# Optimization experiments

Measured on AMD Instinct MI355X. Metric: run time of the kernel, lower is better.

## Reference

```python
import jax, jax.numpy as jnp
import numpy as np

DIM = 768
HEADS = 12
DH = DIM // HEADS
HID = 4 * DIM
EPS = 1e-5


def _layernorm(y, g, b):
    mu = jnp.mean(y, axis=-1, keepdims=True)
    var = jnp.mean(jnp.square(y - mu), axis=-1, keepdims=True)
    return (y - mu) * jax.lax.rsqrt(var + EPS) * g + b


def setup_inputs() -> dict:
    key = jax.random.key(0)
    ks = jax.random.split(key, 8)
    s = 0.02
    return {
        "x": jax.random.normal(ks[0], (8, 1024, DIM), dtype=jnp.float32),
        "Wqkv": jax.random.normal(ks[1], (DIM, 3 * DIM), dtype=jnp.float32) * s,
        "bqkv": jnp.zeros((3 * DIM,), jnp.float32),
        "Wproj": jax.random.normal(ks[2], (DIM, DIM), dtype=jnp.float32) * s,
        "bproj": jnp.zeros((DIM,), jnp.float32),
        "W1": jax.random.normal(ks[3], (DIM, HID), dtype=jnp.float32) * s,
        "b1": jnp.zeros((HID,), jnp.float32),
        "W2": jax.random.normal(ks[4], (HID, DIM), dtype=jnp.float32) * s,
        "b2": jnp.zeros((DIM,), jnp.float32),
        "g1": jnp.ones((DIM,), jnp.float32),
        "be1": jnp.zeros((DIM,), jnp.float32),
        "g2": jnp.ones((DIM,), jnp.float32),
        "be2": jnp.zeros((DIM,), jnp.float32),
    }


def reference(x, Wqkv, bqkv, Wproj, bproj, W1, b1, W2, b2, g1, be1, g2, be2):
    b, n, d = x.shape
    # QKV projection; source splits last dim as (h, d_head, qkv) -> qkv innermost
    qkv = (x @ Wqkv + bqkv).reshape(b, n, HEADS, DH, 3)
    q, k, v = qkv[..., 0], qkv[..., 1], qkv[..., 2]  # [b, n, h, dh]
    scores = jnp.einsum('bqhd,bkhd->bhqk', q, k)
    # NOTE: source applies the 1/sqrt(dim) scale AFTER softmax (quirk preserved)
    attn = jax.nn.softmax(scores, axis=-1) / (d ** 0.5)
    out = jnp.einsum('bhqk,bkhd->bqhd', attn, v).reshape(b, n, d)
    attn_out = out @ Wproj + bproj
    # Residual with norm on the branch output (not pre-norm), per source
    x = x + _layernorm(attn_out, g1, be1)
    mlp_out = jax.nn.gelu(x @ W1 + b1, approximate=False) @ W2 + b2
    return x + _layernorm(mlp_out, g2, be2)
```

## Files before the change

### kernel.cpp

```cpp
#include <hip/hip_runtime.h>
#include <math.h>

typedef float f32x4 __attribute__((ext_vector_type(4)));
typedef short s16x8 __attribute__((ext_vector_type(8)));

#define DIM_ 768
#define HEADS_ 12
#define DH_ 64
#define HID_ 3072
#define SEQ_ 1024
#define BATCH_ 8
#define ROWS_ (BATCH_*SEQ_)

static __device__ __forceinline__ ushort f2bf(float f) {
    union { float f; unsigned u; } v; v.f = f;
    unsigned r = (v.u + 0x7fffu + ((v.u >> 16) & 1u)) >> 16;
    return (ushort)r;
}
static __device__ __forceinline__ float bf2f(ushort u) {
    union { unsigned u; float f; } v; v.u = ((unsigned)u) << 16;
    return v.f;
}

static __device__ __forceinline__ void glds16(const ushort* gp, ushort* lp) {
    __builtin_amdgcn_global_load_lds(
        (const __attribute__((address_space(1))) void*)gp,
        (__attribute__((address_space(3))) void*)lp, 16, 0, 0);
}

__global__ __launch_bounds__(256) void cast_bf16_kernel(
    const float* __restrict__ in, ushort* __restrict__ out, int n4)
{
    int i = blockIdx.x * 256 + threadIdx.x;
    if (i >= n4) return;
    float4 v = ((const float4*)in)[i];
    ushort4 o;
    o.x = f2bf(v.x); o.y = f2bf(v.y); o.z = f2bf(v.z); o.w = f2bf(v.w);
    ((ushort4*)out)[i] = o;
}

__global__ __launch_bounds__(256) void transpose_cast_kernel(
    const float* __restrict__ W, ushort* __restrict__ WT, int K, int N)
{
    __shared__ float tile[32][33];
    int n0 = blockIdx.x * 32, k0 = blockIdx.y * 32;
    int tx = threadIdx.x, ty = threadIdx.y;
#pragma unroll
    for (int i = 0; i < 4; i++)
        tile[ty + i * 8][tx] = W[(size_t)(k0 + ty + i * 8) * N + n0 + tx];
    __syncthreads();
#pragma unroll
    for (int i = 0; i < 4; i++)
        WT[(size_t)(n0 + ty + i * 8) * K + k0 + tx] = f2bf(tile[tx][ty + i * 8]);
}

#define EPI_PART 0
#define EPI_GELU 1
#define EPI_QKV 2

template<int EPI>
__global__ __launch_bounds__(256, 3) void gemm_bt(
    const ushort* __restrict__ A, const ushort* __restrict__ B,
    const float* __restrict__ bias,
    ushort* __restrict__ Cp,
    ushort* __restrict__ Qb, ushort* __restrict__ Kb, ushort* __restrict__ Vt,
    int M, int N, int K, int nx, int nk, int Ksl)
{
    __shared__ ushort As[128 * 64];
    __shared__ ushort Bs[128 * 64];
    const int t = threadIdx.x;
    const int lane = t & 63;
    const int w = t >> 6;
    const int wr = w >> 1, wc = w & 1;
    const int nwg = gridDim.x;
    const int chunk = nwg >> 3;
    const int lin = (blockIdx.x & 7) * chunk + (blockIdx.x >> 3);
    const int tile = lin / nk;
    const int ks = lin - tile * nk;
    const int m0 = (tile / nx) * 128, n0 = (tile % nx) * 128;
    const int lr = lane & 15, g = lane >> 4;

    const ushort* Ak = A + (size_t)ks * Ksl;
    const ushort* Bk = B + (size_t)ks * Ksl;
    const int sr = lane >> 3;
    const int scz = (((lane & 7) ^ sr)) * 8;

    f32x4 acc[4][4] = {};

    for (int k0 = 0; k0 < Ksl; k0 += 64) {
#pragma unroll
        for (int j = 0; j < 4; j++) {
            int r = w * 32 + j * 8;
            glds16(Ak + (size_t)(m0 + r + sr) * K + k0 + scz, &As[r * 64]);
            glds16(Bk + (size_t)(n0 + r + sr) * K + k0 + scz, &Bs[r * 64]);
        }
        __syncthreads();
#pragma unroll
        for (int kk = 0; kk < 2; kk++) {
            s16x8 af[4], bfr[4];
#pragma unroll
            for (int m = 0; m < 4; m++) {
                int row = wr * 64 + m * 16 + lr;
                int slot = (kk * 4 + g) ^ (row & 7);
                af[m] = *(const s16x8*)&As[row * 64 + slot * 8];
            }
#pragma unroll
            for (int n = 0; n < 4; n++) {
                int row = wc * 64 + n * 16 + lr;
                int slot = (kk * 4 + g) ^ (row & 7);
                bfr[n] = *(const s16x8*)&Bs[row * 64 + slot * 8];
            }
#pragma unroll
            for (int m = 0; m < 4; m++)
#pragma unroll
                for (int n = 0; n < 4; n++)
                    acc[m][n] = __builtin_amdgcn_mfma_f32_16x16x32_bf16(af[m], bfr[n], acc[m][n], 0, 0, 0);
        }
        __syncthreads();
    }

    ushort* Cpo = Cp ? Cp + (size_t)ks * M * N : nullptr;
#pragma unroll
    for (int m = 0; m < 4; m++) {
        int row = m0 + wr * 64 + m * 16 + g * 4;
#pragma unroll
        for (int n = 0; n < 4; n++) {
            int col = n0 + wc * 64 + n * 16 + lr;
            float bv = (ks == 0) ? bias[col] : 0.f;
#pragma unroll
            for (int r = 0; r < 4; r++) {
                float v = acc[m][n][r] + bv;
                int rg = row + r;
                if (EPI == EPI_PART) {
                    Cpo[(size_t)rg * N + col] = f2bf(v);
                } else if (EPI == EPI_GELU) {
                    float u = v * (0.7978845608f + 0.0356774081f * v * v);
                    float th = 1.f - 2.f / (__expf(2.f * u) + 1.f);
                    float gl = 0.5f * v * (1.f + th);
                    Cpo[(size_t)rg * N + col] = f2bf(gl);
                } else {
                    int b = rg >> 10, nrow = rg & 1023;
                    int h = col / 192, rem = col % 192;
                    int dh = rem / 3, wh = rem % 3;
                    int hb = b * HEADS_ + h;
                    ushort bw = f2bf(v);
                    if (wh == 0)      Qb[((size_t)hb * SEQ_ + nrow) * DH_ + dh] = bw;
                    else if (wh == 1) Kb[((size_t)hb * SEQ_ + nrow) * DH_ + dh] = bw;
                    else              Vt[(size_t)hb * DH_ * SEQ_ + (size_t)dh * SEQ_ + nrow] = bw;
                }
            }
        }
    }
}

static __device__ __forceinline__ void pack_pv(
    const f32x4 (&S)[4], s16x8& pf0v, s16x8& pf1v)
{
    unsigned c[4][2];
#pragma unroll
    for (int n = 0; n < 4; n++) {
        asm("v_cvt_pk_bf16_f32 %0, %1, %2" : "=v"(c[n][0]) : "v"(S[n][0]), "v"(S[n][1]));
        asm("v_cvt_pk_bf16_f32 %0, %1, %2" : "=v"(c[n][1]) : "v"(S[n][2]), "v"(S[n][3]));
    }
    union { unsigned u[4]; s16x8 v; } pf0, pf1;
#pragma unroll
    for (int m = 0; m < 2; m++) {
        unsigned a = c[0][m], bb = c[1][m];
        asm("v_permlane32_swap_b32 %0, %1" : "+v"(a), "+v"(bb));
        asm("v_permlane16_swap_b32 %0, %1" : "+v"(a), "+v"(bb));
        pf0.u[m] = a; pf0.u[2 + m] = bb;
        unsigned a2 = c[2][m], b2 = c[3][m];
        asm("v_permlane32_swap_b32 %0, %1" : "+v"(a2), "+v"(b2));
        asm("v_permlane16_swap_b32 %0, %1" : "+v"(a2), "+v"(b2));
        pf1.u[m] = a2; pf1.u[2 + m] = b2;
    }
    pf0v = pf0.v; pf1v = pf1.v;
}

struct AttnState {
    s16x8 aqA0, aqA1, aqB0, aqB1;
    float lA, lB;
    f32x4 OA[4], OB[4];
};

static __device__ __forceinline__ void attn_tile_lds(
    AttnState& st, const ushort* Ksb, const ushort* Vsb, int lr, int g)
{
    const float CMAX = 20.f;
    const int x = lr & 7;
    s16x8 kf[8], vf[8];
#pragma unroll
    for (int n = 0; n < 4; n++) {
        int row = n * 16 + lr;
        kf[2 * n]     = *(const s16x8*)&Ksb[row * 64 + (g ^ x) * 8];
        kf[2 * n + 1] = *(const s16x8*)&Ksb[row * 64 + ((4 + g) ^ x) * 8];
        vf[2 * n]     = *(const s16x8*)&Vsb[row * 64 + (g ^ x) * 8];
        vf[2 * n + 1] = *(const s16x8*)&Vsb[row * 64 + ((4 + g) ^ x) * 8];
    }
    f32x4 SA[4] = {}, SB[4] = {};
#pragma unroll
    for (int n = 0; n < 4; n++) {
        SA[n] = __builtin_amdgcn_mfma_f32_16x16x32_bf16(kf[2 * n], st.aqA0, SA[n], 0, 0, 0);
        SA[n] = __builtin_amdgcn_mfma_f32_16x16x32_bf16(kf[2 * n + 1], st.aqA1, SA[n], 0, 0, 0);
    }
#pragma unroll
    for (int n = 0; n < 4; n++) {
        SB[n] = __builtin_amdgcn_mfma_f32_16x16x32_bf16(kf[2 * n], st.aqB0, SB[n], 0, 0, 0);
        SB[n] = __builtin_amdgcn_mfma_f32_16x16x32_bf16(kf[2 * n + 1], st.aqB1, SB[n], 0, 0, 0);
    }
#pragma unroll
    for (int n = 0; n < 4; n++)
#pragma unroll
        for (int r = 0; r < 4; r++) {
            SA[n][r] = __expf(SA[n][r] - CMAX);
            SB[n][r] = __expf(SB[n][r] - CMAX);
        }
    f32x4 sa = SA[0] + SA[1], sb = SB[0] + SB[1];
    sa += SA[2] + SA[3];
    sb += SB[2] + SB[3];
    st.lA += (sa[0] + sa[1]) + (sa[2] + sa[3]);
    st.lB += (sb[0] + sb[1]) + (sb[2] + sb[3]);

    s16x8 pfA0, pfA1, pfB0, pfB1;
    pack_pv(SA, pfA0, pfA1);
    pack_pv(SB, pfB0, pfB1);

#pragma unroll
    for (int n = 0; n < 4; n++) {
        st.OA[n] = __builtin_amdgcn_mfma_f32_16x16x32_bf16(pfA0, vf[2 * n], st.OA[n], 0, 0, 0);
        st.OA[n] = __builtin_amdgcn_mfma_f32_16x16x32_bf16(pfA1, vf[2 * n + 1], st.OA[n], 0, 0, 0);
    }
#pragma unroll
    for (int n = 0; n < 4; n++) {
        st.OB[n] = __builtin_amdgcn_mfma_f32_16x16x32_bf16(pfB0, vf[2 * n], st.OB[n], 0, 0, 0);
        st.OB[n] = __builtin_amdgcn_mfma_f32_16x16x32_bf16(pfB1, vf[2 * n + 1], st.OB[n], 0, 0, 0);
    }
}

__global__ __launch_bounds__(256) void attn_kernel(
    const ushort* __restrict__ Q, const ushort* __restrict__ Kb,
    const ushort* __restrict__ Vt, ushort* __restrict__ AO)
{
    __shared__ ushort Ks[2][64 * 64];
    __shared__ ushort Vs[2][64 * 64];
    const int tid = threadIdx.x, lane = tid & 63, w = tid >> 6;
    const int lr = lane & 15, g = lane >> 4;
    const int wg = blockIdx.x;
    const int lin = (wg & 7) * 96 + (wg >> 3);
    const int bh = lin >> 3;
    const int qt = lin & 7;
    const int b = bh / HEADS_, h = bh % HEADS_;
    const ushort* qh = Q + (size_t)bh * SEQ_ * DH_;
    const ushort* kh = Kb + (size_t)bh * SEQ_ * DH_;
    const ushort* vh = Vt + (size_t)bh * DH_ * SEQ_;

    const int srow = tid >> 3;
    const int ss = (tid & 7) ^ (srow & 7);

    AttnState st;
    const int qbase = qt * 128 + w * 32;
    st.aqA0 = *(const s16x8*)(qh + (size_t)(qbase + lr) * DH_ + g * 8);
    st.aqA1 = *(const s16x8*)(qh + (size_t)(qbase + lr) * DH_ + 32 + g * 8);
    st.aqB0 = *(const s16x8*)(qh + (size_t)(qbase + 16 + lr) * DH_ + g * 8);
    st.aqB1 = *(const s16x8*)(qh + (size_t)(qbase + 16 + lr) * DH_ + 32 + g * 8);
    st.lA = 0.f; st.lB = 0.f;
#pragma unroll
    for (int n = 0; n < 4; n++) { st.OA[n] = f32x4{}; st.OB[n] = f32x4{}; }

    auto stageK = [&](ushort* buf, int kbase) {
        glds16(kh + (size_t)(kbase + srow) * DH_ + ss * 8, &buf[tid * 8]);
        glds16(kh + (size_t)(kbase + 32 + srow) * DH_ + ss * 8, &buf[tid * 8 + 2048]);
    };
    auto stageV = [&](ushort* buf, int kbase) {
        glds16(vh + (size_t)srow * SEQ_ + kbase + ss * 8, &buf[tid * 8]);
        glds16(vh + (size_t)(32 + srow) * SEQ_ + kbase + ss * 8, &buf[tid * 8 + 2048]);
    };

    stageK(Ks[0], 0);
    stageV(Vs[0], 0);
    __syncthreads();

#pragma unroll 1
    for (int tkv = 0; tkv < 16; tkv += 2) {
        if (tkv + 1 < 16) { stageK(Ks[1], (tkv + 1) * 64); stageV(Vs[1], (tkv + 1) * 64); }
        attn_tile_lds(st, Ks[0], Vs[0], lr, g);
        __syncthreads();
        if (tkv + 2 < 16) { stageK(Ks[0], (tkv + 2) * 64); stageV(Vs[0], (tkv + 2) * 64); }
        attn_tile_lds(st, Ks[1], Vs[1], lr, g);
        __syncthreads();
    }

    float lA = st.lA, lB = st.lB;
    lA += __shfl_xor(lA, 16); lA += __shfl_xor(lA, 32);
    lB += __shfl_xor(lB, 16); lB += __shfl_xor(lB, 32);

    const float fin = 0.03608439182435161f;
#pragma unroll
    for (int r = 0; r < 4; r++) {
        float linvA = fin / __shfl(lA, 4 * g + r);
        float linvB = fin / __shfl(lB, 4 * g + r);
        int rowA = b * SEQ_ + qbase + 4 * g + r;
        int rowB = rowA + 16;
        ushort* aoA = AO + (size_t)rowA * DIM_ + h * DH_ + lr;
        ushort* aoB = AO + (size_t)rowB * DIM_ + h * DH_ + lr;
#pragma unroll
        for (int n = 0; n < 4; n++) {
            aoA[n * 16] = f2bf(st.OA[n][r] * linvA);
            aoB[n * 16] = f2bf(st.OB[n][r] * linvB);
        }
    }
}

__global__ __launch_bounds__(256) void ln_residual_kernel(
    const float* __restrict__ xin, const ushort* __restrict__ y0,
    const ushort* __restrict__ y1,
    const float* __restrict__ g, const float* __restrict__ be,
    float* __restrict__ outf, ushort* __restrict__ outbf, int rows)
{
    int w = threadIdx.x >> 6, lane = threadIdx.x & 63;
    int row = blockIdx.x * 4 + w;
    if (row >= rows) return;
    const ushort4* y0r = (const ushort4*)(y0 + (size_t)row * DIM_);
    const ushort4* y1r = y1 ? (const ushort4*)(y1 + (size_t)row * DIM_) : nullptr;
    float4 v[3];
    float s = 0.f, s2 = 0.f;
#pragma unroll
    for (int i = 0; i < 3; i++) {
        ushort4 u0 = y0r[i * 64 + lane];
        float4 a = { bf2f(u0.x), bf2f(u0.y), bf2f(u0.z), bf2f(u0.w) };
        if (y1r) {
            ushort4 u1 = y1r[i * 64 + lane];
            a.x += bf2f(u1.x); a.y += bf2f(u1.y); a.z += bf2f(u1.z); a.w += bf2f(u1.w);
        }
        v[i] = a;
        s += (a.x + a.y) + (a.z + a.w);
        s2 += (a.x * a.x + a.y * a.y) + (a.z * a.z + a.w * a.w);
    }
#pragma unroll
    for (int o = 1; o < 64; o <<= 1) { s += __shfl_xor(s, o); s2 += __shfl_xor(s2, o); }
    float mu = s * (1.f / 768.f);
    float var = s2 * (1.f / 768.f) - mu * mu;
    float rs = rsqrtf(var + 1e-5f);
    const float4* xr = (const float4*)(xin + (size_t)row * DIM_);
    const float4* g4 = (const float4*)g;
    const float4* b4 = (const float4*)be;
    float4* of = (float4*)(outf + (size_t)row * DIM_);
#pragma unroll
    for (int i = 0; i < 3; i++) {
        int c = i * 64 + lane;
        float4 gg = g4[c], bb = b4[c], xx = xr[c];
        float4 o;
        o.x = xx.x + (v[i].x - mu) * rs * gg.x + bb.x;
        o.y = xx.y + (v[i].y - mu) * rs * gg.y + bb.y;
        o.z = xx.z + (v[i].z - mu) * rs * gg.z + bb.z;
        o.w = xx.w + (v[i].w - mu) * rs * gg.w + bb.w;
        of[c] = o;
        if (outbf) {
            ushort4 ob;
            ob.x = f2bf(o.x); ob.y = f2bf(o.y); ob.z = f2bf(o.z); ob.w = f2bf(o.w);
            ((ushort4*)(outbf + (size_t)row * DIM_))[c] = ob;
        }
    }
}

extern "C" void kernel_launch(void* const* d_in, const int* in_sizes, int n_in,
                              void* d_out, int out_size, void* d_ws, size_t ws_size,
                              hipStream_t stream)
{
    const float* x    = (const float*)d_in[0];
    const float* Wqkv = (const float*)d_in[1];
    const float* bqkv = (const float*)d_in[2];
    const float* Wproj= (const float*)d_in[3];
    const float* bproj= (const float*)d_in[4];
    const float* W1   = (const float*)d_in[5];
    const float* b1   = (const float*)d_in[6];
    const float* W2   = (const float*)d_in[7];
    const float* b2   = (const float*)d_in[8];
    const float* g1   = (const float*)d_in[9];
    const float* be1  = (const float*)d_in[10];
    const float* g2   = (const float*)d_in[11];
    const float* be2  = (const float*)d_in[12];
    float* out = (float*)d_out;

    char* ws = (char*)d_ws;
    size_t off = 0;
    auto alloc = [&](size_t bytes) -> void* {
        void* p = ws + off;
        off += (bytes + 255) & ~(size_t)255;
        return p;
    };
    ushort* wqkvT  = (ushort*)alloc((size_t)2304 * 768 * 2);
    ushort* wprojT = (ushort*)alloc((size_t)768 * 768 * 2);
    ushort* w1T    = (ushort*)alloc((size_t)3072 * 768 * 2);
    ushort* w2T    = (ushort*)alloc((size_t)768 * 3072 * 2);
    ushort* xbf    = (ushort*)alloc((size_t)ROWS_ * DIM_ * 2);
    ushort* qb     = (ushort*)alloc((size_t)ROWS_ * DIM_ * 2);
    ushort* kb     = (ushort*)alloc((size_t)ROWS_ * DIM_ * 2);
    ushort* vT     = (ushort*)alloc((size_t)ROWS_ * DIM_ * 2);
    ushort* hbf    = xbf;
    ushort* aobf   = (ushort*)alloc((size_t)ROWS_ * DIM_ * 2);
    ushort* projp  = (ushort*)alloc((size_t)2 * ROWS_ * DIM_ * 2);
    float*  x1f    = (float*) alloc((size_t)ROWS_ * DIM_ * 4);
    ushort* x1bf   = (ushort*)alloc((size_t)ROWS_ * DIM_ * 2);
    ushort* projp1 = projp + (size_t)ROWS_ * DIM_;

    cast_bf16_kernel<<<(ROWS_ * DIM_ / 4 + 255) / 256, 256, 0, stream>>>(x, xbf, ROWS_ * DIM_ / 4);
    transpose_cast_kernel<<<dim3(2304 / 32, 768 / 32), dim3(32, 8), 0, stream>>>(Wqkv, wqkvT, 768, 2304);
    transpose_cast_kernel<<<dim3(768 / 32, 768 / 32), dim3(32, 8), 0, stream>>>(Wproj, wprojT, 768, 768);
    transpose_cast_kernel<<<dim3(3072 / 32, 768 / 32), dim3(32, 8), 0, stream>>>(W1, w1T, 768, 3072);
    transpose_cast_kernel<<<dim3(768 / 32, 3072 / 32), dim3(32, 8), 0, stream>>>(W2, w2T, 3072, 768);

    gemm_bt<EPI_QKV><<<1152, 256, 0, stream>>>(
        xbf, wqkvT, bqkv, nullptr, qb, kb, vT, ROWS_, 2304, 768, 18, 1, 768);

    attn_kernel<<<768, 256, 0, stream>>>(qb, kb, vT, aobf);

    gemm_bt<EPI_PART><<<768, 256, 0, stream>>>(
        aobf, wprojT, bproj, projp, nullptr, nullptr, nullptr, ROWS_, 768, 768, 6, 2, 384);

    ln_residual_kernel<<<ROWS_ / 4, 256, 0, stream>>>(x, projp, projp1, g1, be1, x1f, x1bf, ROWS_);

    gemm_bt<EPI_GELU><<<1536, 256, 0, stream>>>(
        x1bf, w1T, b1, hbf, nullptr, nullptr, nullptr, ROWS_, 3072, 768, 24, 1, 768);

    gemm_bt<EPI_PART><<<768, 256, 0, stream>>>(
        hbf, w2T, b2, projp, nullptr, nullptr, nullptr, ROWS_, 768, 3072, 6, 2, 1536);

    ln_residual_kernel<<<ROWS_ / 4, 256, 0, stream>>>(x1f, projp, projp1, g2, be2, out, nullptr, ROWS_);
}
```

Baseline: 254.0 us.

## Permute QKV weights for contiguous epilogue, drop fp32 residual buffer, raise occupancy

Reorders the QKV weight columns during the transpose-cast so each GEMM tile writes only Q, K or V with contiguous head dims. This removes the per-element div/mod and the scattered stores in the QKV epilogue. The intermediate residual is now kept only in bf16, which removes an fp32 write and read, at the cost of residual precision in the final output. The GEMM launch bound is raised to 4 blocks per CU, which may add register pressure.

```diff
diff --git a/kernel.cpp b/kernel.cpp
--- a/kernel.cpp
+++ b/kernel.cpp
@@ -54,12 +54,30 @@
         WT[(size_t)(n0 + ty + i * 8) * K + k0 + tx] = f2bf(tile[tx][ty + i * 8]);
 }
 
+__global__ __launch_bounds__(256) void transpose_cast_qkv_kernel(
+    const float* __restrict__ W, ushort* __restrict__ WT)
+{
+    __shared__ float tile[32][33];
+    int n0 = blockIdx.x * 32, k0 = blockIdx.y * 32;
+    int tx = threadIdx.x, ty = threadIdx.y;
+    int np = n0 + tx;
+    int part = np / 768, idx = np % 768;
+    int oc = ((idx >> 6) * 192) + ((idx & 63) * 3) + part;
+#pragma unroll
+    for (int i = 0; i < 4; i++)
+        tile[ty + i * 8][tx] = W[(size_t)(k0 + ty + i * 8) * 2304 + oc];
+    __syncthreads();
+#pragma unroll
+    for (int i = 0; i < 4; i++)
+        WT[(size_t)(n0 + ty + i * 8) * 768 + k0 + tx] = f2bf(tile[tx][ty + i * 8]);
+}
+
 #define EPI_PART 0
 #define EPI_GELU 1
 #define EPI_QKV 2
 
 template<int EPI>
-__global__ __launch_bounds__(256, 3) void gemm_bt(
+__global__ __launch_bounds__(256, 4) void gemm_bt(
     const ushort* __restrict__ A, const ushort* __restrict__ B,
     const float* __restrict__ bias,
     ushort* __restrict__ Cp,
@@ -120,13 +138,22 @@
     }
 
     ushort* Cpo = Cp ? Cp + (size_t)ks * M * N : nullptr;
+    const int part = (EPI == EPI_QKV) ? (n0 / 768) : 0;
 #pragma unroll
     for (int m = 0; m < 4; m++) {
         int row = m0 + wr * 64 + m * 16 + g * 4;
 #pragma unroll
         for (int n = 0; n < 4; n++) {
             int col = n0 + wc * 64 + n * 16 + lr;
-            float bv = (ks == 0) ? bias[col] : 0.f;
+            float bv;
+            int h = 0, dh = 0;
+            if (EPI == EPI_QKV) {
+                int idx = col - part * 768;
+                h = idx >> 6; dh = idx & 63;
+                bv = bias[h * 192 + dh * 3 + part];
+            } else {
+                bv = (ks == 0) ? bias[col] : 0.f;
+            }
 #pragma unroll
             for (int r = 0; r < 4; r++) {
                 float v = acc[m][n][r] + bv;
@@ -140,13 +167,11 @@
                     Cpo[(size_t)rg * N + col] = f2bf(gl);
                 } else {
                     int b = rg >> 10, nrow = rg & 1023;
-                    int h = col / 192, rem = col % 192;
-                    int dh = rem / 3, wh = rem % 3;
                     int hb = b * HEADS_ + h;
                     ushort bw = f2bf(v);
-                    if (wh == 0)      Qb[((size_t)hb * SEQ_ + nrow) * DH_ + dh] = bw;
-                    else if (wh == 1) Kb[((size_t)hb * SEQ_ + nrow) * DH_ + dh] = bw;
-                    else              Vt[(size_t)hb * DH_ * SEQ_ + (size_t)dh * SEQ_ + nrow] = bw;
+                    if (part == 0)      Qb[((size_t)hb * SEQ_ + nrow) * DH_ + dh] = bw;
+                    else if (part == 1) Kb[((size_t)hb * SEQ_ + nrow) * DH_ + dh] = bw;
+                    else                Vt[(size_t)hb * DH_ * SEQ_ + (size_t)dh * SEQ_ + nrow] = bw;
                 }
             }
         }
@@ -312,8 +337,8 @@
 }
 
 __global__ __launch_bounds__(256) void ln_residual_kernel(
-    const float* __restrict__ xin, const ushort* __restrict__ y0,
-    const ushort* __restrict__ y1,
+    const float* __restrict__ xinf, const ushort* __restrict__ xinb,
+    const ushort* __restrict__ y0, const ushort* __restrict__ y1,
     const float* __restrict__ g, const float* __restrict__ be,
     float* __restrict__ outf, ushort* __restrict__ outbf, int rows)
 {
@@ -341,20 +366,27 @@
     float mu = s * (1.f / 768.f);
     float var = s2 * (1.f / 768.f) - mu * mu;
     float rs = rsqrtf(var + 1e-5f);
-    const float4* xr = (const float4*)(xin + (size_t)row * DIM_);
+    const float4* xr = xinf ? (const float4*)(xinf + (size_t)row * DIM_) : nullptr;
+    const ushort4* xb = xinb ? (const ushort4*)(xinb + (size_t)row * DIM_) : nullptr;
     const float4* g4 = (const float4*)g;
     const float4* b4 = (const float4*)be;
-    float4* of = (float4*)(outf + (size_t)row * DIM_);
+    float4* of = outf ? (float4*)(outf + (size_t)row * DIM_) : nullptr;
 #pragma unroll
     for (int i = 0; i < 3; i++) {
         int c = i * 64 + lane;
-        float4 gg = g4[c], bb = b4[c], xx = xr[c];
+        float4 gg = g4[c], bb = b4[c];
+        float4 xx;
+        if (xr) xx = xr[c];
+        else {
+            ushort4 u = xb[c];
+            xx = { bf2f(u.x), bf2f(u.y), bf2f(u.z), bf2f(u.w) };
+        }
         float4 o;
         o.x = xx.x + (v[i].x - mu) * rs * gg.x + bb.x;
         o.y = xx.y + (v[i].y - mu) * rs * gg.y + bb.y;
         o.z = xx.z + (v[i].z - mu) * rs * gg.z + bb.z;
         o.w = xx.w + (v[i].w - mu) * rs * gg.w + bb.w;
-        of[c] = o;
+        if (of) of[c] = o;
         if (outbf) {
             ushort4 ob;
             ob.x = f2bf(o.x); ob.y = f2bf(o.y); ob.z = f2bf(o.z); ob.w = f2bf(o.w);
@@ -400,12 +432,11 @@
     ushort* hbf    = xbf;
     ushort* aobf   = (ushort*)alloc((size_t)ROWS_ * DIM_ * 2);
     ushort* projp  = (ushort*)alloc((size_t)2 * ROWS_ * DIM_ * 2);
-    float*  x1f    = (float*) alloc((size_t)ROWS_ * DIM_ * 4);
     ushort* x1bf   = (ushort*)alloc((size_t)ROWS_ * DIM_ * 2);
     ushort* projp1 = projp + (size_t)ROWS_ * DIM_;
 
     cast_bf16_kernel<<<(ROWS_ * DIM_ / 4 + 255) / 256, 256, 0, stream>>>(x, xbf, ROWS_ * DIM_ / 4);
-    transpose_cast_kernel<<<dim3(2304 / 32, 768 / 32), dim3(32, 8), 0, stream>>>(Wqkv, wqkvT, 768, 2304);
+    transpose_cast_qkv_kernel<<<dim3(2304 / 32, 768 / 32), dim3(32, 8), 0, stream>>>(Wqkv, wqkvT);
     transpose_cast_kernel<<<dim3(768 / 32, 768 / 32), dim3(32, 8), 0, stream>>>(Wproj, wprojT, 768, 768);
     transpose_cast_kernel<<<dim3(3072 / 32, 768 / 32), dim3(32, 8), 0, stream>>>(W1, w1T, 768, 3072);
     transpose_cast_kernel<<<dim3(768 / 32, 3072 / 32), dim3(32, 8), 0, stream>>>(W2, w2T, 3072, 768);
@@ -418,7 +449,8 @@
     gemm_bt<EPI_PART><<<768, 256, 0, stream>>>(
         aobf, wprojT, bproj, projp, nullptr, nullptr, nullptr, ROWS_, 768, 768, 6, 2, 384);
 
-    ln_residual_kernel<<<ROWS_ / 4, 256, 0, stream>>>(x, projp, projp1, g1, be1, x1f, x1bf, ROWS_);
+    ln_residual_kernel<<<ROWS_ / 4, 256, 0, stream>>>(
+        x, nullptr, projp, projp1, g1, be1, nullptr, x1bf, ROWS_);
 
     gemm_bt<EPI_GELU><<<1536, 256, 0, stream>>>(
         x1bf, w1T, b1, hbf, nullptr, nullptr, nullptr, ROWS_, 3072, 768, 24, 1, 768);
@@ -426,5 +458,6 @@
     gemm_bt<EPI_PART><<<768, 256, 0, stream>>>(
         hbf, w2T, b2, projp, nullptr, nullptr, nullptr, ROWS_, 768, 3072, 6, 2, 1536);
 
-    ln_residual_kernel<<<ROWS_ / 4, 256, 0, stream>>>(x1f, projp, projp1, g2, be2, out, nullptr, ROWS_);
-}
+    ln_residual_kernel<<<ROWS_ / 4, 256, 0, stream>>>(
+        nullptr, x1bf, projp, projp1, g2, be2, out, nullptr, ROWS_);
+}
```

After: 250.1 us. No clear change (-1.5%).
